# Performance work log

Hardware: AMD Instinct MI355X
Metric: run time of the kernel (lower is better)

Reference implementation:

```python
import jax, jax.numpy as jnp
import numpy as np

B, S, HID = 2, 1024, 1024
H, P, D = 16, 2, 64
SCALE = 1.0 / np.sqrt(D)


def setup_inputs() -> dict:
    key = jax.random.key(0)
    ks = jax.random.split(key, 9)
    hidden_states = jax.random.normal(ks[0], (B, S, HID), dtype=jnp.float32)
    w_std = 0.02
    Wq = jax.random.normal(ks[1], (HID, HID), dtype=jnp.float32) * w_std
    Wk = jax.random.normal(ks[2], (HID, HID), dtype=jnp.float32) * w_std
    Wv = jax.random.normal(ks[3], (HID, HID), dtype=jnp.float32) * w_std
    Wo = jax.random.normal(ks[4], (HID, HID), dtype=jnp.float32) * w_std
    # alpha_* initialized as identity over heads, broadcast over pseudo dim, plus noise
    ident = jnp.broadcast_to(jnp.eye(H, dtype=jnp.float32)[:, :, None], (H, H, P))
    alpha_q = ident + 0.01 * jax.random.normal(ks[5], (H, H, P), dtype=jnp.float32)
    alpha_k = ident + 0.01 * jax.random.normal(ks[6], (H, H, P), dtype=jnp.float32)
    alpha_v = ident + 0.01 * jax.random.normal(ks[7], (H, H, P), dtype=jnp.float32)
    # collapse: (H, H*P), one-hot picking pseudo-head 0 of each head, plus noise
    collapse = jnp.zeros((H, H * P), dtype=jnp.float32)
    hi = jnp.arange(H)
    collapse = collapse.at[hi, hi * P].set(1.0)
    collapse = collapse + 0.01 * jax.random.normal(ks[8], (H, H * P), dtype=jnp.float32)
    return {"hidden_states": hidden_states, "Wq": Wq, "Wk": Wk, "Wv": Wv, "Wo": Wo,
            "alpha_q": alpha_q, "alpha_k": alpha_k, "alpha_v": alpha_v, "collapse": collapse}


def _iha_forward(x, Wq, Wk, Wv, Wo, alpha_q, alpha_k, alpha_v, collapse):
    b, s, _ = x.shape
    # projections (torch F.linear: x @ W^T), split into heads -> (b, H, s, D)
    def proj(W):
        return jnp.einsum('bse,fe->bsf', x, W).reshape(b, s, H, D).transpose(0, 2, 1, 3)
    q, k, v = proj(Wq), proj(Wk), proj(Wv)
    # head mixing: mhp,bmnd->bhpnd then merge pseudo into virtual seq (b,H,s*P,D)
    def mix_merge(alpha, t):
        t = jnp.einsum('mhp,bmnd->bhpnd', alpha, t)
        return t.transpose(0, 1, 3, 2, 4).reshape(b, H, s * P, D)
    q, k, v = mix_merge(alpha_q, q), mix_merge(alpha_k, k), mix_merge(alpha_v, v)
    # causal SDPA over virtual positions
    sv = s * P
    scores = jnp.einsum('bhqd,bhkd->bhqk', q, k) * jnp.asarray(SCALE, x.dtype)
    vpos = jnp.arange(sv)
    causal = vpos[:, None] >= vpos[None, :]
    scores = jnp.where(causal, scores, jnp.asarray(-jnp.inf, x.dtype))
    probs = jax.nn.softmax(scores, axis=-1)
    attn = jnp.einsum('bhqk,bhkd->bhqd', probs, v)  # (b, H, sv, D)
    # collapse pseudo heads: (b,H,s,P,D) -> (b,s,H*P,D) -> einsum with collapse
    attn = attn.reshape(b, H, s, P, D).transpose(0, 2, 1, 3, 4).reshape(b, s, H * P, D)
    attn = jnp.einsum('ho,bnod->bhnd', collapse, attn)  # (b, H, s, D)
    attn = attn.transpose(0, 2, 1, 3).reshape(b, s, HID)
    return jnp.einsum('bse,fe->bsf', attn, Wo)


def reference(hidden_states, Wq, Wk, Wv, Wo, alpha_q, alpha_k, alpha_v, collapse):
    return _iha_forward(hidden_states, Wq, Wk, Wv, Wo, alpha_q, alpha_k, alpha_v, collapse)
```

## Files before the change

### kernel.cpp

```cpp
#include <hip/hip_runtime.h>
#include <hip/hip_bf16.h>

#define B_    2
#define S_    1024
#define HID_  1024
#define H_    16
#define P_    2
#define D_    64
#define SV_   2048
#define NBH_  32
#define SCALE_LOG2E 0.18033688f

typedef __attribute__((ext_vector_type(8))) short short8;
typedef __attribute__((ext_vector_type(4))) short short4b;
typedef __attribute__((ext_vector_type(4))) float f32x4;

#if __has_builtin(__builtin_amdgcn_exp2f)
#define EXP2(x) __builtin_amdgcn_exp2f(x)
#else
#define EXP2(x) exp2f(x)
#endif

__device__ __forceinline__ unsigned short f2bf(float f) {
  union { float f; unsigned u; } v; v.f = f;
  unsigned r = v.u + 0x7fffu + ((v.u >> 16) & 1u);
  return (unsigned short)(r >> 16);
}
__device__ __forceinline__ unsigned pack_bf2(float a, float b) {
  __hip_bfloat162 h = __float22bfloat162_rn(make_float2(a, b));
  unsigned u; __builtin_memcpy(&u, &h, 4);
  return u;
}

__global__ __launch_bounds__(256) void cast_f32_bf16(
    const float* __restrict__ src, unsigned short* __restrict__ dst, int n4) {
  int i = blockIdx.x * blockDim.x + threadIdx.x;
  int stride = gridDim.x * blockDim.x;
  for (; i < n4; i += stride) {
    float4 v = ((const float4*)src)[i];
    ushort4 o;
    o.x = f2bf(v.x); o.y = f2bf(v.y); o.z = f2bf(v.z); o.w = f2bf(v.w);
    ((ushort4*)dst)[i] = o;
  }
}

__global__ __launch_bounds__(256) void weff_kernel(
    const float* __restrict__ Wq, const float* __restrict__ Wk,
    const float* __restrict__ Wv,
    const float* __restrict__ aq, const float* __restrict__ ak,
    const float* __restrict__ av,
    unsigned short* __restrict__ Weff) {
  __shared__ float Al[16][32];
  const int d = blockIdx.x;
  const int t = blockIdx.y;
  const float* W = (t == 0) ? Wq : ((t == 1) ? Wk : Wv);
  const float* A = (t == 0) ? aq : ((t == 1) ? ak : av);
  const int tid = threadIdx.x;
  for (int idx = tid; idx < 512; idx += 256) Al[idx >> 5][idx & 31] = A[idx];
  __syncthreads();
  const int e = tid * 4;
  float wr[16][4];
#pragma unroll
  for (int m = 0; m < 16; ++m) {
    float4 v = *(const float4*)(W + (size_t)(m * 64 + d) * 1024 + e);
    wr[m][0] = v.x; wr[m][1] = v.y; wr[m][2] = v.z; wr[m][3] = v.w;
  }
  for (int hp = 0; hp < 32; ++hp) {
    float acc0 = 0.f, acc1 = 0.f, acc2 = 0.f, acc3 = 0.f;
#pragma unroll
    for (int m = 0; m < 16; ++m) {
      float al = Al[m][hp];
      acc0 += al * wr[m][0]; acc1 += al * wr[m][1];
      acc2 += al * wr[m][2]; acc3 += al * wr[m][3];
    }
    int r = (hp >> 1) * 128 + (hp & 1) * 64 + d;
    ushort4 ov;
    ov.x = f2bf(acc0); ov.y = f2bf(acc1); ov.z = f2bf(acc2); ov.w = f2bf(acc3);
    *(ushort4*)(Weff + ((size_t)t * 2048 + r) * 1024 + e) = ov;
  }
}

__global__ __launch_bounds__(256) void woeff_kernel(
    const float* __restrict__ Wo, const float* __restrict__ coll,
    unsigned short* __restrict__ Woeff) {
  __shared__ float wrow[1024];
  __shared__ float cl[512];
  const int f = blockIdx.x;
  const int tid = threadIdx.x;
  for (int idx = tid; idx < 512; idx += 256) cl[idx] = coll[idx];
  for (int idx = tid; idx < 1024; idx += 256) wrow[idx] = Wo[(size_t)f * 1024 + idx];
  __syncthreads();
  for (int idx = tid; idx < 2048; idx += 256) {
    int o = idx >> 6, d = idx & 63;
    float acc = 0.f;
#pragma unroll
    for (int h = 0; h < 16; ++h) acc += wrow[h * 64 + d] * cl[h * 32 + o];
    Woeff[(size_t)f * 2048 + idx] = f2bf(acc);
  }
}

__global__ __launch_bounds__(512) void qkv_gemm256(
    const unsigned short* __restrict__ Xb,
    const unsigned short* __restrict__ Weff,
    unsigned short* __restrict__ Qd, unsigned short* __restrict__ Kd,
    unsigned short* __restrict__ Vd) {
  __shared__ unsigned short As[3][256 * 64];
  __shared__ unsigned short Bs[2][256 * 64];
  constexpr int K = 1024;
  constexpr int NT = 16;
  const int t = threadIdx.x;
  const int wave = t >> 6, lane = t & 63, lrow = lane & 15, quad = lane >> 4;
  const int wm = wave >> 2, wn = wave & 3;
  const int z = blockIdx.z;
  const int row0 = blockIdx.x * 256, col0 = blockIdx.y * 256;
  const unsigned short* Ap = (z == 2) ? (Weff + (size_t)2 * 2048 * 1024) : Xb;
  const unsigned short* Bp = (z == 2) ? Xb : (Weff + (size_t)z * 2048 * 1024);

  const int srow8 = lane >> 3;
  const int sslot = (lane & 7) ^ srow8;

  auto stageHT = [&](const unsigned short* __restrict__ gsrc,
                     unsigned short* __restrict__ ldsbase,
                     int half, int kt, int trow0) {
#pragma unroll
    for (int j = 0; j < 2; ++j) {
      const int rloc = half * 128 + wave * 16 + j * 8;
      const unsigned short* g =
          gsrc + (size_t)(trow0 + rloc + srow8) * K + kt * 64 + sslot * 8;
      __builtin_amdgcn_global_load_lds(
          (const __attribute__((address_space(1))) unsigned int*)g,
          (__attribute__((address_space(3))) unsigned int*)(ldsbase + rloc * 64),
          16, 0, 0);
    }
  };

  f32x4 acc[8][4];
#pragma unroll
  for (int mi = 0; mi < 8; ++mi)
#pragma unroll
    for (int ni = 0; ni < 4; ++ni) acc[mi][ni] = (f32x4){0.f, 0.f, 0.f, 0.f};

  stageHT(Ap, &As[0][0], 0, 0, row0);
  stageHT(Ap, &As[0][0], 1, 0, row0);
  stageHT(Bp, &Bs[0][0], 0, 0, col0);
  stageHT(Bp, &Bs[0][0], 1, 0, col0);
  stageHT(Ap, &As[1][0], 0, 1, row0);
  stageHT(Ap, &As[1][0], 1, 1, row0);
  stageHT(Bp, &Bs[1][0], 0, 1, col0);
  stageHT(Bp, &Bs[1][0], 1, 1, col0);
  asm volatile("s_waitcnt vmcnt(8)" ::: "memory");
  asm volatile("s_barrier" ::: "memory");

  const int swz = lrow & 7;

#define LDA(mi, ks)                                                         \
  (*(const short8*)(Ab + (wm * 128 + (mi)*16 + lrow) * 64 +                 \
                    ((((ks)*4 + quad) ^ swz) * 8)))

#define MFMA_PAIR(mA, mB, a00, a01, a10, a11)                               \
  _Pragma("unroll") for (int ni = 0; ni < 4; ++ni) {                        \
    acc[mA][ni] = __builtin_amdgcn_mfma_f32_16x16x32_bf16(                  \
        a00, bfrag[ni][0], acc[mA][ni], 0, 0, 0);                           \
    acc[mA][ni] = __builtin_amdgcn_mfma_f32_16x16x32_bf16(                  \
        a01, bfrag[ni][1], acc[mA][ni], 0, 0, 0);                           \
    acc[mB][ni] = __builtin_amdgcn_mfma_f32_16x16x32_bf16(                  \
        a10, bfrag[ni][0], acc[mB][ni], 0, 0, 0);                           \
    acc[mB][ni] = __builtin_amdgcn_mfma_f32_16x16x32_bf16(                  \
        a11, bfrag[ni][1], acc[mB][ni], 0, 0, 0);                           \
  }

  for (int kt = 0; kt < NT; ++kt) {
    const int abuf = kt % 3;
    const int anext = (kt + 2) % 3;
    const int bbuf = kt & 1;
    const bool pf = (kt + 2 < NT);
    const unsigned short* __restrict__ Ab = &As[abuf][0];
    const unsigned short* __restrict__ Bb = &Bs[bbuf][0];

    short8 bfrag[4][2];
    {
#pragma unroll
      for (int ni = 0; ni < 4; ++ni) {
        const int R = wn * 64 + ni * 16 + lrow;
#pragma unroll
        for (int ks = 0; ks < 2; ++ks)
          bfrag[ni][ks] =
              *(const short8*)(Bb + R * 64 + (((ks * 4 + quad) ^ swz) * 8));
      }
      short8 a00 = LDA(0, 0), a01 = LDA(0, 1), a10 = LDA(1, 0), a11 = LDA(1, 1);
      if (pf) stageHT(Ap, &As[anext][0], 0, kt + 2, row0);
      asm volatile("s_barrier" ::: "memory");
      asm volatile("s_waitcnt lgkmcnt(0)" ::: "memory");
      __builtin_amdgcn_s_setprio(1);
      MFMA_PAIR(0, 1, a00, a01, a10, a11)
      __builtin_amdgcn_s_setprio(0);
      asm volatile("s_barrier" ::: "memory");
    }
    {
      short8 a00 = LDA(2, 0), a01 = LDA(2, 1), a10 = LDA(3, 0), a11 = LDA(3, 1);
      if (pf) stageHT(Ap, &As[anext][0], 1, kt + 2, row0);
      asm volatile("s_barrier" ::: "memory");
      asm volatile("s_waitcnt lgkmcnt(0)" ::: "memory");
      __builtin_amdgcn_s_setprio(1);
      MFMA_PAIR(2, 3, a00, a01, a10, a11)
      __builtin_amdgcn_s_setprio(0);
      asm volatile("s_barrier" ::: "memory");
    }
    {
      short8 a00 = LDA(4, 0), a01 = LDA(4, 1), a10 = LDA(5, 0), a11 = LDA(5, 1);
      if (pf) stageHT(Bp, &Bs[bbuf][0], 0, kt + 2, col0);
      asm volatile("s_barrier" ::: "memory");
      asm volatile("s_waitcnt lgkmcnt(0)" ::: "memory");
      __builtin_amdgcn_s_setprio(1);
      MFMA_PAIR(4, 5, a00, a01, a10, a11)
      __builtin_amdgcn_s_setprio(0);
      asm volatile("s_barrier" ::: "memory");
    }
    {
      short8 a00 = LDA(6, 0), a01 = LDA(6, 1), a10 = LDA(7, 0), a11 = LDA(7, 1);
      if (pf) stageHT(Bp, &Bs[bbuf][0], 1, kt + 2, col0);
      asm volatile("s_barrier" ::: "memory");
      asm volatile("s_waitcnt lgkmcnt(0)" ::: "memory");
      __builtin_amdgcn_s_setprio(1);
      MFMA_PAIR(6, 7, a00, a01, a10, a11)
      __builtin_amdgcn_s_setprio(0);
      if (pf) {
        asm volatile("s_waitcnt vmcnt(8)" ::: "memory");
      } else {
        asm volatile("s_waitcnt vmcnt(0)" ::: "memory");
      }
      asm volatile("s_barrier" ::: "memory");
    }
  }
#undef LDA
#undef MFMA_PAIR

#pragma unroll
  for (int mi = 0; mi < 8; ++mi) {
#pragma unroll
    for (int ni = 0; ni < 4; ++ni) {
#pragma unroll
      for (int i = 0; i < 4; ++i) {
        int grow = row0 + wm * 128 + mi * 16 + quad * 4 + i;
        int gcol = col0 + wn * 64 + ni * 16 + lrow;
        float val = acc[mi][ni][i];
        if (z != 2) {
          if (z == 0) val *= SCALE_LOG2E;
          int b = grow >> 10, n = grow & 1023;
          int h = gcol >> 7, p = (gcol >> 6) & 1, d = gcol & 63;
          unsigned short* dst = (z == 0) ? Qd : Kd;
          dst[((size_t)((b * 16 + h) * 2048) + n * 2 + p) * 64 + d] = f2bf(val);
        } else {
          int h = grow >> 7, p = (grow >> 6) & 1, d = grow & 63;
          int b = gcol >> 10, n = gcol & 1023;
          Vd[((size_t)((b * 16 + h) * 64 + d)) * 2048 + n * 2 + p] = f2bf(val);
        }
      }
    }
  }
}

__global__ __launch_bounds__(256) void gemm64(
    const unsigned short* __restrict__ A,
    const unsigned short* __restrict__ Bbase,
    int M, int N, int K, float* __restrict__ Cf) {
  __shared__ unsigned short As[2][64 * 32];
  __shared__ unsigned short Bs[2][128 * 32];
  const int t = threadIdx.x;
  const int wave = t >> 6, lane = t & 63, lrow = lane & 15, quad = lane >> 4;
  const int row0 = blockIdx.x * 64;
  const int col0 = blockIdx.y * 128;

  const int r16 = lane >> 2;
  const int gc = (lane & 3) * 8;

  auto stage = [&](int k0, int buf) {
    const unsigned short* ga = A + (size_t)(row0 + wave * 16 + r16) * K + k0 + gc;
    __builtin_amdgcn_global_load_lds(
        (const __attribute__((address_space(1))) unsigned int*)ga,
        (__attribute__((address_space(3))) unsigned int*)(&As[buf][wave * 512]), 16, 0, 0);
#pragma unroll
    for (int j = 0; j < 2; ++j) {
      const int cc = wave * 2 + j;
      const unsigned short* gb = Bbase + (size_t)(col0 + cc * 16 + r16) * K + k0 + gc;
      __builtin_amdgcn_global_load_lds(
          (const __attribute__((address_space(1))) unsigned int*)gb,
          (__attribute__((address_space(3))) unsigned int*)(&Bs[buf][cc * 512]), 16, 0, 0);
    }
  };

  f32x4 acc[4][2];
#pragma unroll
  for (int mi = 0; mi < 4; ++mi)
#pragma unroll
    for (int ni = 0; ni < 2; ++ni) acc[mi][ni] = (f32x4){0.f, 0.f, 0.f, 0.f};

  const int niter = K >> 5;
  stage(0, 0);

  for (int it = 0; it < niter; ++it) {
    const int buf = it & 1;
    if (it + 1 < niter) {
      stage((it + 1) * 32, buf ^ 1);
      asm volatile("s_waitcnt vmcnt(3)" ::: "memory");
    } else {
      asm volatile("s_waitcnt vmcnt(0)" ::: "memory");
    }
    asm volatile("s_barrier" ::: "memory");

    short8 af[4], bfr[2];
#pragma unroll
    for (int mi = 0; mi < 4; ++mi)
      af[mi] = *(const short8*)(&As[buf][(mi * 16 + lrow) * 32 + quad * 8]);
#pragma unroll
    for (int ni = 0; ni < 2; ++ni)
      bfr[ni] = *(const short8*)(&Bs[buf][(wave * 32 + ni * 16 + lrow) * 32 + quad * 8]);
#pragma unroll
    for (int mi = 0; mi < 4; ++mi)
#pragma unroll
      for (int ni = 0; ni < 2; ++ni)
        acc[mi][ni] = __builtin_amdgcn_mfma_f32_16x16x32_bf16(af[mi], bfr[ni],
                                                              acc[mi][ni], 0, 0, 0);

    asm volatile("s_barrier" ::: "memory");
  }

#pragma unroll
  for (int mi = 0; mi < 4; ++mi)
#pragma unroll
    for (int ni = 0; ni < 2; ++ni)
#pragma unroll
      for (int i = 0; i < 4; ++i) {
        int grow = row0 + mi * 16 + quad * 4 + i;
        int gcol = col0 + wave * 32 + ni * 16 + lrow;
        Cf[(size_t)grow * N + gcol] = acc[mi][ni][i];
      }
}

__global__ __launch_bounds__(256, 4) void attn_kernel(
    const unsigned short* __restrict__ Qv, const unsigned short* __restrict__ Kv,
    const unsigned short* __restrict__ Vt, unsigned short* __restrict__ Aov) {
  __shared__ unsigned short Ks[2][4096];
  __shared__ unsigned short Vs[2][4096];
  const int bh = blockIdx.x;
  const int yy = blockIdx.y;
  const int qt = (yy < 16) ? yy : (47 - yy);
  const int t = threadIdx.x;
  const int w = t >> 6, lane = t & 63, lq = lane & 15, quad = lane >> 4;
  const int l3 = lq & 7;

  const unsigned short* Qh = Qv + (size_t)bh * SV_ * D_;
  const unsigned short* Kh = Kv + (size_t)bh * SV_ * D_;
  const unsigned short* Vh = Vt + (size_t)bh * D_ * SV_;

  const int qrow = qt * 64 + w * 16 + lq;
  short8 bq0 = *(const short8*)(Qh + (size_t)qrow * 64 + quad * 8);
  short8 bq1 = *(const short8*)(Qh + (size_t)qrow * 64 + 32 + quad * 8);

  const int sg = (lane & 7) ^ ((lane >> 3) & 7);
  const int r0 = w * 16 + (lane >> 3);
  const unsigned short* Kg0 = Kh + r0 * 64 + sg * 8;
  const unsigned short* Vg0 = Vh + (size_t)r0 * SV_ + sg * 8;
  const int lds0 = w * 1024;
  const int lds1 = lds0 + 512;

  auto stage = [&](int kt) {
    const int buf = kt & 1;
    const unsigned short* kg = Kg0 + kt * 4096;
    const unsigned short* vg = Vg0 + kt * 64;
    __builtin_amdgcn_global_load_lds(
        (const __attribute__((address_space(1))) unsigned int*)kg,
        (__attribute__((address_space(3))) unsigned int*)(&Ks[buf][lds0]), 16, 0, 0);
    __builtin_amdgcn_global_load_lds(
        (const __attribute__((address_space(1))) unsigned int*)(kg + 8 * 64),
        (__attribute__((address_space(3))) unsigned int*)(&Ks[buf][lds1]), 16, 0, 0);
    __builtin_amdgcn_global_load_lds(
        (const __attribute__((address_space(1))) unsigned int*)vg,
        (__attribute__((address_space(3))) unsigned int*)(&Vs[buf][lds0]), 16, 0, 0);
    __builtin_amdgcn_global_load_lds(
        (const __attribute__((address_space(1))) unsigned int*)(vg + (size_t)8 * SV_),
        (__attribute__((address_space(3))) unsigned int*)(&Vs[buf][lds1]), 16, 0, 0);
  };

  float l_sum = 0.f;
  f32x4 o_acc[4];
#pragma unroll
  for (int nd = 0; nd < 4; ++nd) o_acc[nd] = (f32x4){0.f, 0.f, 0.f, 0.f};

  const int nt = qt + 1;
  stage(0);

  for (int kt = 0; kt < nt; ++kt) {
    const int buf = kt & 1;
    if (kt + 1 < nt) {
      stage(kt + 1);
      asm volatile("s_waitcnt vmcnt(4)" ::: "memory");
    } else {
      asm volatile("s_waitcnt vmcnt(0)" ::: "memory");
    }
    asm volatile("s_barrier" ::: "memory");

    const unsigned short* Kb = Ks[buf];
    short8 ka[4][2];
#pragma unroll
    for (int t4 = 0; t4 < 4; ++t4)
#pragma unroll
      for (int c = 0; c < 2; ++c)
        ka[t4][c] = *(const short8*)(Kb + (t4 * 16 + lq) * 64 + (((c * 4 + quad) ^ l3) * 8));

    f32x4 s[4];
#pragma unroll
    for (int t4 = 0; t4 < 4; ++t4) {
      f32x4 z = (f32x4){0.f, 0.f, 0.f, 0.f};
      z = __builtin_amdgcn_mfma_f32_16x16x32_bf16(ka[t4][0], bq0, z, 0, 0, 0);
      s[t4] = __builtin_amdgcn_mfma_f32_16x16x32_bf16(ka[t4][1], bq1, z, 0, 0, 0);
    }

    const bool diag = (kt == qt);
    const int kc0 = kt * 64 + quad * 4;
    const unsigned short* Vb = Vs[buf];
    float rs = 0.f;
#pragma unroll
    for (int t4 = 0; t4 < 4; ++t4) {
      float p[4];
#pragma unroll
      for (int i = 0; i < 4; ++i) {
        float e = EXP2(s[t4][i]);
        if (diag) e = (kc0 + t4 * 16 + i > qrow) ? 0.f : e;
        p[i] = e;
        rs += e;
      }
      unsigned ww[2];
      ww[0] = pack_bf2(p[0], p[1]);
      ww[1] = pack_bf2(p[2], p[3]);
      short4b pb;
      __builtin_memcpy(&pb, ww, 8);
      const int cg = t4 * 2 + (quad >> 1);
      const int vcol = ((cg ^ l3) * 8) + (quad & 1) * 4;
#pragma unroll
      for (int nd = 0; nd < 4; ++nd) {
        short4b va4;
        __builtin_memcpy(&va4, Vb + (nd * 16 + lq) * 64 + vcol, 8);
        o_acc[nd] = __builtin_amdgcn_mfma_f32_16x16x16bf16_1k(va4, pb,
                                                              o_acc[nd], 0, 0, 0);
      }
    }
    l_sum += rs;

    asm volatile("s_barrier" ::: "memory");
  }

  l_sum += __shfl_xor(l_sum, 16);
  l_sum += __shfl_xor(l_sum, 32);

  const int b = bh >> 4, h = bh & 15;
  const float inv = 1.0f / l_sum;
  const int n = qrow >> 1, p = qrow & 1;
  unsigned short* dst = Aov + ((size_t)(b * 1024 + n)) * 2048 + (h * 2 + p) * 64;
#pragma unroll
  for (int nd = 0; nd < 4; ++nd) {
    uint2 dw;
    dw.x = pack_bf2(o_acc[nd][0] * inv, o_acc[nd][1] * inv);
    dw.y = pack_bf2(o_acc[nd][2] * inv, o_acc[nd][3] * inv);
    *(uint2*)(dst + nd * 16 + quad * 4) = dw;
  }
}

extern "C" void kernel_launch(void* const* d_in, const int* in_sizes, int n_in,
                              void* d_out, int out_size, void* d_ws, size_t ws_size,
                              hipStream_t stream) {
  (void)in_sizes; (void)n_in; (void)out_size; (void)ws_size;
  const float* x    = (const float*)d_in[0];
  const float* Wq   = (const float*)d_in[1];
  const float* Wk   = (const float*)d_in[2];
  const float* Wv   = (const float*)d_in[3];
  const float* Wo   = (const float*)d_in[4];
  const float* aq   = (const float*)d_in[5];
  const float* ak   = (const float*)d_in[6];
  const float* av   = (const float*)d_in[7];
  const float* coll = (const float*)d_in[8];
  float* out = (float*)d_out;

  char* ws = (char*)d_ws;
  const size_t MB = 1024 * 1024;
  unsigned short* Xb    = (unsigned short*)(ws);
  unsigned short* Woeff = (unsigned short*)(ws + 4 * MB);
  unsigned short* Weff  = (unsigned short*)(ws + 8 * MB);
  unsigned short* Qv    = (unsigned short*)(ws + 20 * MB);
  unsigned short* Kv    = (unsigned short*)(ws + 28 * MB);
  unsigned short* Vt    = (unsigned short*)(ws + 36 * MB);
  unsigned short* Aov   = (unsigned short*)(ws + 8 * MB);

  cast_f32_bf16<<<dim3(1024), dim3(256), 0, stream>>>(x, Xb, (B_ * S_ * HID_) / 4);
  weff_kernel<<<dim3(64, 3), dim3(256), 0, stream>>>(Wq, Wk, Wv, aq, ak, av, Weff);
  qkv_gemm256<<<dim3(8, 8, 3), dim3(512), 0, stream>>>(Xb, Weff, Qv, Kv, Vt);
  attn_kernel<<<dim3(32, 32), dim3(256), 0, stream>>>(Qv, Kv, Vt, Aov);
  woeff_kernel<<<dim3(1024), dim3(256), 0, stream>>>(Wo, coll, Woeff);
  gemm64<<<dim3(32, 8), dim3(256), 0, stream>>>(
      Aov, Woeff, 2048, 1024, 2048, out);
}
```

Baseline: 206.8 us.

## Retile output GEMM with triple buffering; use 128-key register-staged attention tiles

The output projection GEMM moves to 64x64 tiles with a K-step of 64, three LDS buffers, XOR-swizzled LDS layout and MFMA priority boosting, which doubles the grid. The attention kernel now processes 128-key tiles through a single LDS buffer filled from registers, prefetching the next tile into registers while computing, and halves the number of barriered iterations. The aim is fewer synchronisations and better overlap of memory loads with MFMA work. In exchange, even query tiles compute a partly masked half tile, and there is more register pressure from the staged loads.

```diff
diff --git a/kernel.cpp b/kernel.cpp
--- a/kernel.cpp
+++ b/kernel.cpp
@@ -260,79 +260,95 @@
   }
 }
 
-__global__ __launch_bounds__(256) void gemm64(
+__global__ __launch_bounds__(256) void gemm64p(
     const unsigned short* __restrict__ A,
     const unsigned short* __restrict__ Bbase,
-    int M, int N, int K, float* __restrict__ Cf) {
-  __shared__ unsigned short As[2][64 * 32];
-  __shared__ unsigned short Bs[2][128 * 32];
+    float* __restrict__ Cf) {
+  __shared__ unsigned short As[3][64 * 64];
+  __shared__ unsigned short Bs[3][64 * 64];
+  constexpr int K = 2048, N = 1024, NT = 32;
   const int t = threadIdx.x;
   const int wave = t >> 6, lane = t & 63, lrow = lane & 15, quad = lane >> 4;
-  const int row0 = blockIdx.x * 64;
-  const int col0 = blockIdx.y * 128;
-
-  const int r16 = lane >> 2;
-  const int gc = (lane & 3) * 8;
-
-  auto stage = [&](int k0, int buf) {
-    const unsigned short* ga = A + (size_t)(row0 + wave * 16 + r16) * K + k0 + gc;
-    __builtin_amdgcn_global_load_lds(
-        (const __attribute__((address_space(1))) unsigned int*)ga,
-        (__attribute__((address_space(3))) unsigned int*)(&As[buf][wave * 512]), 16, 0, 0);
+  const int wm = wave >> 1, wn = wave & 1;
+  const int row0 = blockIdx.x * 64, col0 = blockIdx.y * 64;
+  const int srow8 = lane >> 3;
+  const int sslot = (lane & 7) ^ srow8;
+  const int swz = lrow & 7;
+
+  auto stage = [&](int kt, int buf) {
 #pragma unroll
     for (int j = 0; j < 2; ++j) {
-      const int cc = wave * 2 + j;
-      const unsigned short* gb = Bbase + (size_t)(col0 + cc * 16 + r16) * K + k0 + gc;
+      const int rloc = wave * 16 + j * 8;
+      const unsigned short* ga =
+          A + (size_t)(row0 + rloc + srow8) * K + kt * 64 + sslot * 8;
+      __builtin_amdgcn_global_load_lds(
+          (const __attribute__((address_space(1))) unsigned int*)ga,
+          (__attribute__((address_space(3))) unsigned int*)(&As[buf][rloc * 64]),
+          16, 0, 0);
+      const unsigned short* gb =
+          Bbase + (size_t)(col0 + rloc + srow8) * K + kt * 64 + sslot * 8;
       __builtin_amdgcn_global_load_lds(
           (const __attribute__((address_space(1))) unsigned int*)gb,
-          (__attribute__((address_space(3))) unsigned int*)(&Bs[buf][cc * 512]), 16, 0, 0);
+          (__attribute__((address_space(3))) unsigned int*)(&Bs[buf][rloc * 64]),
+          16, 0, 0);
     }
   };
 
-  f32x4 acc[4][2];
-#pragma unroll
-  for (int mi = 0; mi < 4; ++mi)
+  f32x4 acc[2][2];
+#pragma unroll
+  for (int mi = 0; mi < 2; ++mi)
 #pragma unroll
     for (int ni = 0; ni < 2; ++ni) acc[mi][ni] = (f32x4){0.f, 0.f, 0.f, 0.f};
 
-  const int niter = K >> 5;
   stage(0, 0);
-
-  for (int it = 0; it < niter; ++it) {
-    const int buf = it & 1;
-    if (it + 1 < niter) {
-      stage((it + 1) * 32, buf ^ 1);
-      asm volatile("s_waitcnt vmcnt(3)" ::: "memory");
+  stage(1, 1);
+
+  for (int kt = 0; kt < NT; ++kt) {
+    const int buf = kt % 3;
+    if (kt < NT - 1) {
+      asm volatile("s_waitcnt vmcnt(4)" ::: "memory");
     } else {
       asm volatile("s_waitcnt vmcnt(0)" ::: "memory");
     }
     asm volatile("s_barrier" ::: "memory");
-
-    short8 af[4], bfr[2];
-#pragma unroll
-    for (int mi = 0; mi < 4; ++mi)
-      af[mi] = *(const short8*)(&As[buf][(mi * 16 + lrow) * 32 + quad * 8]);
+    if (kt + 2 < NT) stage(kt + 2, (kt + 2) % 3);
+
+    const unsigned short* __restrict__ Ab = &As[buf][0];
+    const unsigned short* __restrict__ Bb = &Bs[buf][0];
+    short8 af[2][2], bf[2][2];
+#pragma unroll
+    for (int mi = 0; mi < 2; ++mi)
+#pragma unroll
+      for (int ks = 0; ks < 2; ++ks)
+        af[mi][ks] = *(const short8*)(
+            Ab + (wm * 32 + mi * 16 + lrow) * 64 + (((ks * 4 + quad) ^ swz) * 8));
 #pragma unroll
     for (int ni = 0; ni < 2; ++ni)
-      bfr[ni] = *(const short8*)(&Bs[buf][(wave * 32 + ni * 16 + lrow) * 32 + quad * 8]);
-#pragma unroll
-    for (int mi = 0; mi < 4; ++mi)
-#pragma unroll
-      for (int ni = 0; ni < 2; ++ni)
-        acc[mi][ni] = __builtin_amdgcn_mfma_f32_16x16x32_bf16(af[mi], bfr[ni],
-                                                              acc[mi][ni], 0, 0, 0);
-
-    asm volatile("s_barrier" ::: "memory");
-  }
-
-#pragma unroll
-  for (int mi = 0; mi < 4; ++mi)
+#pragma unroll
+      for (int ks = 0; ks < 2; ++ks)
+        bf[ni][ks] = *(const short8*)(
+            Bb + (wn * 32 + ni * 16 + lrow) * 64 + (((ks * 4 + quad) ^ swz) * 8));
+    __builtin_amdgcn_s_setprio(1);
+#pragma unroll
+    for (int mi = 0; mi < 2; ++mi)
+#pragma unroll
+      for (int ni = 0; ni < 2; ++ni) {
+        acc[mi][ni] = __builtin_amdgcn_mfma_f32_16x16x32_bf16(
+            af[mi][0], bf[ni][0], acc[mi][ni], 0, 0, 0);
+        acc[mi][ni] = __builtin_amdgcn_mfma_f32_16x16x32_bf16(
+            af[mi][1], bf[ni][1], acc[mi][ni], 0, 0, 0);
+      }
+    __builtin_amdgcn_s_setprio(0);
+  }
+
+#pragma unroll
+  for (int mi = 0; mi < 2; ++mi)
 #pragma unroll
     for (int ni = 0; ni < 2; ++ni)
 #pragma unroll
       for (int i = 0; i < 4; ++i) {
-        int grow = row0 + mi * 16 + quad * 4 + i;
-        int gcol = col0 + wave * 32 + ni * 16 + lrow;
+        int grow = row0 + wm * 32 + mi * 16 + quad * 4 + i;
+        int gcol = col0 + wn * 32 + ni * 16 + lrow;
         Cf[(size_t)grow * N + gcol] = acc[mi][ni][i];
       }
 }
@@ -340,8 +356,8 @@
 __global__ __launch_bounds__(256, 4) void attn_kernel(
     const unsigned short* __restrict__ Qv, const unsigned short* __restrict__ Kv,
     const unsigned short* __restrict__ Vt, unsigned short* __restrict__ Aov) {
-  __shared__ unsigned short Ks[2][4096];
-  __shared__ unsigned short Vs[2][4096];
+  __shared__ unsigned short Ks[128 * 64];
+  __shared__ unsigned short Vs[64 * 128];
   const int bh = blockIdx.x;
   const int yy = blockIdx.y;
   const int qt = (yy < 16) ? yy : (47 - yy);
@@ -357,29 +373,29 @@
   short8 bq0 = *(const short8*)(Qh + (size_t)qrow * 64 + quad * 8);
   short8 bq1 = *(const short8*)(Qh + (size_t)qrow * 64 + 32 + quad * 8);
 
-  const int sg = (lane & 7) ^ ((lane >> 3) & 7);
-  const int r0 = w * 16 + (lane >> 3);
-  const unsigned short* Kg0 = Kh + r0 * 64 + sg * 8;
-  const unsigned short* Vg0 = Vh + (size_t)r0 * SV_ + sg * 8;
-  const int lds0 = w * 1024;
-  const int lds1 = lds0 + 512;
-
-  auto stage = [&](int kt) {
-    const int buf = kt & 1;
-    const unsigned short* kg = Kg0 + kt * 4096;
-    const unsigned short* vg = Vg0 + kt * 64;
-    __builtin_amdgcn_global_load_lds(
-        (const __attribute__((address_space(1))) unsigned int*)kg,
-        (__attribute__((address_space(3))) unsigned int*)(&Ks[buf][lds0]), 16, 0, 0);
-    __builtin_amdgcn_global_load_lds(
-        (const __attribute__((address_space(1))) unsigned int*)(kg + 8 * 64),
-        (__attribute__((address_space(3))) unsigned int*)(&Ks[buf][lds1]), 16, 0, 0);
-    __builtin_amdgcn_global_load_lds(
-        (const __attribute__((address_space(1))) unsigned int*)vg,
-        (__attribute__((address_space(3))) unsigned int*)(&Vs[buf][lds0]), 16, 0, 0);
-    __builtin_amdgcn_global_load_lds(
-        (const __attribute__((address_space(1))) unsigned int*)(vg + (size_t)8 * SV_),
-        (__attribute__((address_space(3))) unsigned int*)(&Vs[buf][lds1]), 16, 0, 0);
+  const int krow = t >> 1;
+  const int kslot0 = (t & 1) * 4;
+  const int vrow = t >> 2;
+  const int vslot0 = (t & 3) * 4;
+  const unsigned short* Kgl = Kh + (size_t)krow * 64 + kslot0 * 8;
+  const unsigned short* Vgl = Vh + (size_t)vrow * SV_ + vslot0 * 8;
+
+  int kw_addr[4], vw_addr[4];
+#pragma unroll
+  for (int q = 0; q < 4; ++q) {
+    const int ks = kslot0 + q;
+    kw_addr[q] = krow * 128 + ((ks ^ (krow & 7)) * 16);
+    const int vs = vslot0 + q;
+    vw_addr[q] = vrow * 256 + (((vs & 8) | ((vs & 7) ^ (vrow & 7))) * 16);
+  }
+
+  int4 kreg[4], vreg[4];
+  auto load_tile = [&](int i) {
+#pragma unroll
+    for (int q = 0; q < 4; ++q) {
+      kreg[q] = *(const int4*)(Kgl + (size_t)i * 8192 + q * 8);
+      vreg[q] = *(const int4*)(Vgl + i * 128 + q * 8);
+    }
   };
 
   float l_sum = 0.f;
@@ -387,47 +403,40 @@
 #pragma unroll
   for (int nd = 0; nd < 4; ++nd) o_acc[nd] = (f32x4){0.f, 0.f, 0.f, 0.f};
 
-  const int nt = qt + 1;
-  stage(0);
-
-  for (int kt = 0; kt < nt; ++kt) {
-    const int buf = kt & 1;
-    if (kt + 1 < nt) {
-      stage(kt + 1);
-      asm volatile("s_waitcnt vmcnt(4)" ::: "memory");
-    } else {
-      asm volatile("s_waitcnt vmcnt(0)" ::: "memory");
-    }
-    asm volatile("s_barrier" ::: "memory");
-
-    const unsigned short* Kb = Ks[buf];
-    short8 ka[4][2];
-#pragma unroll
-    for (int t4 = 0; t4 < 4; ++t4)
-#pragma unroll
-      for (int c = 0; c < 2; ++c)
-        ka[t4][c] = *(const short8*)(Kb + (t4 * 16 + lq) * 64 + (((c * 4 + quad) ^ l3) * 8));
-
-    f32x4 s[4];
-#pragma unroll
-    for (int t4 = 0; t4 < 4; ++t4) {
+  const int nt128 = (qt >> 1) + 1;
+  load_tile(0);
+
+  for (int i = 0; i < nt128; ++i) {
+    __builtin_amdgcn_s_barrier();
+    asm volatile("s_waitcnt vmcnt(0)" ::: "memory");
+#pragma unroll
+    for (int q = 0; q < 4; ++q)
+      *(int4*)((char*)Ks + kw_addr[q]) = kreg[q];
+#pragma unroll
+    for (int q = 0; q < 4; ++q)
+      *(int4*)((char*)Vs + vw_addr[q]) = vreg[q];
+    if (i + 1 < nt128) load_tile(i + 1);
+    asm volatile("s_waitcnt lgkmcnt(0)" ::: "memory");
+    __builtin_amdgcn_s_barrier();
+
+    const bool diag = (i == nt128 - 1);
+    float rs = 0.f;
+    __builtin_amdgcn_s_setprio(1);
+#pragma unroll
+    for (int t8 = 0; t8 < 8; ++t8) {
+      short8 k0 = *(const short8*)(&Ks[0] + (t8 * 16 + lq) * 64 + (((0 * 4 + quad) ^ l3) * 8));
+      short8 k1 = *(const short8*)(&Ks[0] + (t8 * 16 + lq) * 64 + (((1 * 4 + quad) ^ l3) * 8));
       f32x4 z = (f32x4){0.f, 0.f, 0.f, 0.f};
-      z = __builtin_amdgcn_mfma_f32_16x16x32_bf16(ka[t4][0], bq0, z, 0, 0, 0);
-      s[t4] = __builtin_amdgcn_mfma_f32_16x16x32_bf16(ka[t4][1], bq1, z, 0, 0, 0);
-    }
-
-    const bool diag = (kt == qt);
-    const int kc0 = kt * 64 + quad * 4;
-    const unsigned short* Vb = Vs[buf];
-    float rs = 0.f;
-#pragma unroll
-    for (int t4 = 0; t4 < 4; ++t4) {
+      z = __builtin_amdgcn_mfma_f32_16x16x32_bf16(k0, bq0, z, 0, 0, 0);
+      z = __builtin_amdgcn_mfma_f32_16x16x32_bf16(k1, bq1, z, 0, 0, 0);
+
       float p[4];
 #pragma unroll
-      for (int i = 0; i < 4; ++i) {
-        float e = EXP2(s[t4][i]);
-        if (diag) e = (kc0 + t4 * 16 + i > qrow) ? 0.f : e;
-        p[i] = e;
+      for (int ii = 0; ii < 4; ++ii) {
+        float e = EXP2(z[ii]);
+        if (diag)
+          e = (i * 128 + t8 * 16 + quad * 4 + ii > qrow) ? 0.f : e;
+        p[ii] = e;
         rs += e;
       }
       unsigned ww[2];
@@ -435,19 +444,19 @@
       ww[1] = pack_bf2(p[2], p[3]);
       short4b pb;
       __builtin_memcpy(&pb, ww, 8);
-      const int cg = t4 * 2 + (quad >> 1);
-      const int vcol = ((cg ^ l3) * 8) + (quad & 1) * 4;
+
+      const int vg = t8 * 2 + (quad >> 1);
+      const int vbyte = ((vg & 8) | ((vg & 7) ^ l3)) * 16 + (quad & 1) * 8;
 #pragma unroll
       for (int nd = 0; nd < 4; ++nd) {
         short4b va4;
-        __builtin_memcpy(&va4, Vb + (nd * 16 + lq) * 64 + vcol, 8);
+        __builtin_memcpy(&va4, (const char*)Vs + (nd * 16 + lq) * 256 + vbyte, 8);
         o_acc[nd] = __builtin_amdgcn_mfma_f32_16x16x16bf16_1k(va4, pb,
                                                               o_acc[nd], 0, 0, 0);
       }
     }
+    __builtin_amdgcn_s_setprio(0);
     l_sum += rs;
-
-    asm volatile("s_barrier" ::: "memory");
   }
 
   l_sum += __shfl_xor(l_sum, 16);
@@ -496,6 +505,5 @@
   qkv_gemm256<<<dim3(8, 8, 3), dim3(512), 0, stream>>>(Xb, Weff, Qv, Kv, Vt);
   attn_kernel<<<dim3(32, 32), dim3(256), 0, stream>>>(Qv, Kv, Vt, Aov);
   woeff_kernel<<<dim3(1024), dim3(256), 0, stream>>>(Wo, coll, Woeff);
-  gemm64<<<dim3(32, 8), dim3(256), 0, stream>>>(
-      Aov, Woeff, 2048, 1024, 2048, out);
-}
+  gemm64p<<<dim3(32, 16), dim3(256), 0, stream>>>(Aov, Woeff, out);
+}
```

Measured after the change: 262.8 us. 27.1% more time.
